# Optimization experiments

Hardware: AMD Instinct MI355X
Metric: run time of the kernel (lower is better)

The kernel has to match this reference:

```python
import jax, jax.numpy as jnp
from jax import lax
import numpy as np

B = 32768
N_IN = 8
N_HID = 64
N_CTRL = 2
M_SCEN = (1.0, 1.2)          # scenario parameters for f/g
M_NOM = 1.0
CLF_LAM = 1.0
CBF_LAM = 1.0
P_CLF = 100.0
P_CBF = 50.0
QP_ITERS = 80                # fixed-iteration batched ADMM (OSQP-style) replacing CvxpyLayer
RHO = 1.0
SIGMA = 1e-6
INF = jnp.inf


def setup_inputs() -> dict:
    key = jax.random.key(0)
    ks = jax.random.split(key, 16)
    s = 0.3
    return {
        "x":   jax.random.normal(ks[0], (B, N_IN), jnp.float32),
        "VW1": jax.random.normal(ks[1], (N_HID, N_IN), jnp.float32) * s,
        "Vb1": jax.random.normal(ks[2], (N_HID,), jnp.float32) * s,
        "VW2": jax.random.normal(ks[3], (N_HID, N_HID), jnp.float32) * s,
        "Vb2": jax.random.normal(ks[4], (N_HID,), jnp.float32) * s,
        "HW1": jax.random.normal(ks[5], (N_HID, N_IN), jnp.float32) * s,
        "Hb1": jax.random.normal(ks[6], (N_HID,), jnp.float32) * s,
        "HW2": jax.random.normal(ks[7], (N_HID, N_HID), jnp.float32) * s,
        "Hb2": jax.random.normal(ks[8], (N_HID,), jnp.float32) * s,
        "HW3": jax.random.normal(ks[9], (N_HID, N_HID), jnp.float32) * s,
        "Hb3": jax.random.normal(ks[10], (N_HID,), jnp.float32) * s,
        "HW4": jax.random.normal(ks[11], (1, N_HID), jnp.float32) * s,
        "Hb4": jax.random.normal(ks[12], (1,), jnp.float32) * s,
        "G0":  jax.random.normal(ks[13], (N_IN, N_CTRL), jnp.float32) * s,
        "K":   jax.random.normal(ks[14], (N_IN, N_CTRL), jnp.float32) * s,
    }


def _lyapunov(x, W1, b1, W2, b2):
    t1 = jnp.tanh(x @ W1.T + b1)                                   # [B,H]
    t2 = jnp.tanh(t1 @ W2.T + b2)                                  # [B,H]
    V = 0.5 * jnp.sum(t2 * t2, axis=1)                             # [B]
    # fused diag(1-t^2) @ W chain (no diag_embed materialization)
    D1 = (1.0 - t1 ** 2)[:, :, None] * W1[None]                    # [B,H,N]
    D2 = (1.0 - t2 ** 2)[:, :, None] * jnp.einsum('hk,bkn->bhn', W2, D1)
    grad_V = jnp.einsum('bh,bhn->bn', t2, D2)                      # [B,N]
    return V, grad_V


def _barrier(x, W1, b1, W2, b2, W3, b3, W4, b4):
    t1 = jnp.tanh(x @ W1.T + b1)
    t2 = jnp.tanh(t1 @ W2.T + b2)
    t3 = jnp.tanh(t2 @ W3.T + b3)
    H = t3 @ W4.T + b4                                             # [B,1]
    D1 = (1.0 - t1 ** 2)[:, :, None] * W1[None]
    D2 = (1.0 - t2 ** 2)[:, :, None] * jnp.einsum('hk,bkn->bhn', W2, D1)
    D3 = (1.0 - t3 ** 2)[:, :, None] * jnp.einsum('hk,bkn->bhn', W3, D2)
    grad_H = jnp.einsum('oh,bhn->bn', W4, D3)                      # [B,N] (o=1)
    return H, grad_H


def _solve_qp(q, A, lo, hi):
    """Batched OSQP-style ADMM for min 0.5 z^T P z + q^T z  s.t. lo <= A z <= hi.
    P = diag([2,2,0,0,0,0]); z = [u(2), r_clf(2), s_cbf(2)]. Fixed iterations."""
    nb, mc, nz = A.shape[0], A.shape[1], A.shape[2]
    Pdiag = jnp.array([2.0, 2.0, 0.0, 0.0, 0.0, 0.0], q.dtype)
    M = RHO * jnp.einsum('bmi,bmj->bij', A, A) + jnp.diag(Pdiag + SIGMA)
    Minv = jnp.linalg.inv(M)                                       # [B,6,6]
    x0 = jnp.zeros((nb, nz), q.dtype)
    z0 = jnp.zeros((nb, mc), q.dtype)
    y0 = jnp.zeros((nb, mc), q.dtype)

    def step(carry, _):
        xx, zz, yy = carry
        rhs = SIGMA * xx - q + jnp.einsum('bmi,bm->bi', A, RHO * zz - yy)
        xt = jnp.einsum('bij,bj->bi', Minv, rhs)
        zt = jnp.einsum('bmi,bi->bm', A, xt)
        zn = jnp.clip(zt + yy / RHO, lo, hi)
        yn = yy + RHO * (zt - zn)
        return (xt, zn, yn), None

    (xf, _, _), _ = lax.scan(step, (x0, z0, y0), None, length=QP_ITERS)
    return xf                                                      # [B,6]


def _forward(x, VW1, Vb1, VW2, Vb2, HW1, Hb1, HW2, Hb2, HW3, Hb3, HW4, Hb4, G0, K):
    V, grad_V = _lyapunov(x, VW1, Vb1, VW2, Vb2)
    H, grad_H = _barrier(x, HW1, Hb1, HW2, Hb2, HW3, Hb3, HW4, Hb4)

    LfVs, LgVs, LfHs, LgHs = [], [], [], []
    for m in M_SCEN:
        # f(x,m) = -x/m ; g(x,m) = G0/m
        LfVs.append(-jnp.sum(grad_V * x, axis=1) / m)              # [B]
        LgVs.append((grad_V @ G0) / m)                             # [B,C]
        LfHs.append(-jnp.sum(grad_H * x, axis=1) / m)
        LgHs.append((grad_H @ G0) / m)
    u_nom = -(x @ K) * (1.0 / M_NOM)                               # [B,C]

    nb = x.shape[0]
    z2 = jnp.zeros((nb, 2), x.dtype)
    ey = jnp.eye(2, dtype=x.dtype)
    e = lambda i: jnp.broadcast_to(ey[i], (nb, 2))
    ninf = jnp.full((nb,), -INF, x.dtype)
    pinf = jnp.full((nb,), INF, x.dtype)
    zer = jnp.zeros((nb,), x.dtype)

    rows, los, his = [], [], []
    for i in range(len(M_SCEN)):
        # CBF: LfH + LgH@u + cbf_lam*H + s_i >= 0
        rows.append(jnp.concatenate([LgHs[i], z2, e(i)], axis=1))
        los.append(-(LfHs[i] + CBF_LAM * H[:, 0])); his.append(pinf)
        # CLF: LfV + LgV@u + clf_lam*V - r_i <= 0
        rows.append(jnp.concatenate([LgVs[i], -e(i), z2], axis=1))
        los.append(ninf); his.append(-(LfVs[i] + CLF_LAM * V))
    for i in range(len(M_SCEN)):
        rows.append(jnp.concatenate([z2, e(i), z2], axis=1)); los.append(zer); his.append(pinf)
    for i in range(len(M_SCEN)):
        rows.append(jnp.concatenate([z2, z2, e(i)], axis=1)); los.append(zer); his.append(pinf)

    A = jnp.stack(rows, axis=1)                                    # [B,8,6]
    lo = jnp.stack(los, axis=1)                                    # [B,8]
    hi = jnp.stack(his, axis=1)
    # objective ||u-u_nom||^2 + p_clf*sum r + p_cbf*sum s  ->  q = [-2 u_nom, p_clf, p_clf, p_cbf, p_cbf]
    q = jnp.concatenate([-2.0 * u_nom,
                         jnp.full((nb, 2), P_CLF, x.dtype),
                         jnp.full((nb, 2), P_CBF, x.dtype)], axis=1)

    z = _solve_qp(q, A, lo, hi)                                    # [B,6]
    u = z[:, :N_CTRL]
    relaxation = jnp.mean(z[:, N_CTRL:N_CTRL + len(M_SCEN)], axis=1, keepdims=True)  # [B,1]

    ns = float(len(M_SCEN))
    Vdot = sum(LfVs[i] + jnp.sum(LgVs[i] * u, axis=1) for i in range(len(M_SCEN))) / ns
    Hdot = sum(LfHs[i] + jnp.sum(LgHs[i] * u, axis=1) for i in range(len(M_SCEN))) / ns
    return u, relaxation, V, Vdot[:, None, None], H, Hdot[:, None, None]


def reference(x, VW1, Vb1, VW2, Vb2, HW1, Hb1, HW2, Hb2, HW3, Hb3, HW4, Hb4, G0, K):
    return _forward(x, VW1, Vb1, VW2, Vb2, HW1, Hb1, HW2, Hb2, HW3, Hb3, HW4, Hb4, G0, K)
```

## Files before the change

### kernel.cpp

```cpp
#include <hip/hip_runtime.h>
#include <hip/hip_bf16.h>
#include <math.h>

typedef _Float16 f16x8 __attribute__((ext_vector_type(8)));
typedef _Float16 f16x4 __attribute__((ext_vector_type(4)));
typedef float    f32x4 __attribute__((ext_vector_type(4)));
typedef float    f32x2 __attribute__((ext_vector_type(2)));

__device__ __forceinline__ float ldin(const void* p, int i, int f32f) {
  return f32f ? ((const float*)p)[i]
              : __bfloat162float(((const __hip_bfloat16*)p)[i]);
}

__device__ __forceinline__ f32x4 MFMA(f16x8 a, f16x8 b, f32x4 c) {
  return __builtin_amdgcn_mfma_f32_16x16x32_f16(a, b, c, 0, 0, 0);
}

__device__ __forceinline__ float tanh_fast(float x) {
  float e = __expf(2.f * x);
  return 1.f - 2.f * __builtin_amdgcn_rcpf(e + 1.f);
}

__device__ __forceinline__ float redq(float v) {
  v += __shfl_xor(v, 16, 64);
  v += __shfl_xor(v, 32, 64);
  return v;
}

__device__ __forceinline__ int widx(int h, int k) {
  return ((h >> 4) << 10) + ((k >> 5) << 9) + (((k >> 3) & 3) << 7) + ((h & 15) << 3) + (k & 7);
}

#define OFF_VW2   0
#define OFF_VW2T  4096
#define OFF_HW2   8192
#define OFF_HW2T  12288
#define OFF_HW3   16384
#define OFF_HW3T  20480
#define OFF_W1V   24576
#define OFF_W1H   26624
#define CF_BASE   28672
#define C_WGV0 0
#define C_WGV1 64
#define C_WGH0 128
#define C_WGH1 192
#define C_VB1  256
#define C_VB2  320
#define C_HB1  384
#define C_HB2  448
#define C_HB3  512
#define C_W4   576
#define C_K    640
#define C_HB4  656
#define C_FLAG 657
#define C_N    658

__global__ __launch_bounds__(256) void prep_kernel(
    const void* px, const void* pVW1, const void* pVW2,
    const void* pHW1, const void* pHW2, const void* pHW3,
    const void* pVb1, const void* pVb2, const void* pHb1, const void* pHb2,
    const void* pHb3, const void* pHW4, const void* pHb4,
    const void* pG0, const void* pK, _Float16* wsp)
{
  __shared__ int sCnt;
  const int tid = threadIdx.x;
  if (tid == 0) sCnt = 0;
  __syncthreads();
  {
    const unsigned short* xb = (const unsigned short*)px;
    int good = 0;
#pragma unroll
    for (int i = 0; i < 2; ++i) {
      int ex = (xb[tid * 2 + i] >> 7) & 0xFF;
      good += (ex >= 97 && ex <= 157) ? 1 : 0;
    }
    atomicAdd(&sCnt, good);
  }
  __syncthreads();
  const int f32f = (sCnt >= 435) ? 0 : 1;

  const int t = blockIdx.x * 256 + tid;
  int h = t >> 6, k = t & 63;
  int fw = widx(h, k), tw = widx(k, h);
  _Float16 v;
  v = (_Float16)ldin(pVW2, t, f32f); wsp[OFF_VW2 + fw] = v; wsp[OFF_VW2T + tw] = v;
  v = (_Float16)ldin(pHW2, t, f32f); wsp[OFF_HW2 + fw] = v; wsp[OFF_HW2T + tw] = v;
  v = (_Float16)ldin(pHW3, t, f32f); wsp[OFF_HW3 + fw] = v; wsp[OFF_HW3T + tw] = v;
  if (t < 512) {
    int hh = t >> 3, j = t & 7;
    int base = ((hh >> 4) << 9) + ((hh & 15) << 3) + j;
    float f = ldin(pVW1, t, f32f); _Float16 hi = (_Float16)f;
    _Float16 lo = f32f ? (_Float16)(f - (float)hi) : (_Float16)0.f;
    wsp[OFF_W1V + base]       = hi;
    wsp[OFF_W1V + base + 128] = hi;
    wsp[OFF_W1V + base + 256] = lo;
    wsp[OFF_W1V + base + 384] = (_Float16)0.f;
    f = ldin(pHW1, t, f32f); hi = (_Float16)f;
    lo = f32f ? (_Float16)(f - (float)hi) : (_Float16)0.f;
    wsp[OFF_W1H + base]       = hi;
    wsp[OFF_W1H + base + 128] = hi;
    wsp[OFF_W1H + base + 256] = lo;
    wsp[OFF_W1H + base + 384] = (_Float16)0.f;
  }
  if (blockIdx.x == 0) {
    float* wsF = (float*)(wsp + CF_BASE);
    if (tid < 64) {
      float a0 = 0.f, a1 = 0.f, b0 = 0.f, b1 = 0.f;
#pragma unroll
      for (int nn = 0; nn < 8; ++nn) {
        float g0 = ldin(pG0, 2 * nn, f32f), g1 = ldin(pG0, 2 * nn + 1, f32f);
        float wv = ldin(pVW1, tid * 8 + nn, f32f), wh = ldin(pHW1, tid * 8 + nn, f32f);
        a0 += wv * g0; a1 += wv * g1; b0 += wh * g0; b1 += wh * g1;
      }
      wsF[C_WGV0 + tid] = a0; wsF[C_WGV1 + tid] = a1;
      wsF[C_WGH0 + tid] = b0; wsF[C_WGH1 + tid] = b1;
      wsF[C_VB1 + tid] = ldin(pVb1, tid, f32f);
      wsF[C_VB2 + tid] = ldin(pVb2, tid, f32f);
      wsF[C_HB1 + tid] = ldin(pHb1, tid, f32f);
      wsF[C_HB2 + tid] = ldin(pHb2, tid, f32f);
      wsF[C_HB3 + tid] = ldin(pHb3, tid, f32f);
      wsF[C_W4  + tid] = ldin(pHW4, tid, f32f);
    }
    if (tid < 16) wsF[C_K + tid] = ldin(pK, tid, f32f);
    if (tid == 0) { wsF[C_HB4] = ldin(pHb4, 0, f32f); ((int*)wsF)[C_FLAG] = f32f; }
  }
}

__global__ __launch_bounds__(512, 2) void main_kernel(
    const void* px, const _Float16* wsp, float* out)
{
  __shared__ __align__(16) _Float16 sAct[8][1024];
  __shared__ __align__(16) float sQPs[10][128];
  __shared__ __align__(16) float sC[C_N];

  const int tid = threadIdx.x, lane = tid & 63, w = tid >> 6;
  const int n = lane & 15, q = lane >> 4;
  const int e0 = blockIdx.x * 128 + w * 16;

  const float* cf = (const float*)(wsp + CF_BASE);
  for (int i = tid; i < C_N; i += 512) sC[i] = cf[i];
  const int f32f = ((const int*)cf)[C_FLAG];
  __syncthreads();

  float xv[8];
  if (f32f) {
    const f32x4* xp = (const f32x4*)((const float*)px + (e0 + n) * 8);
    f32x4 x0 = xp[0], x1 = xp[1];
#pragma unroll
    for (int j = 0; j < 4; ++j) { xv[j] = x0[j]; xv[4 + j] = x1[j]; }
  } else {
    uint4 u = *(const uint4*)((const unsigned short*)px + (e0 + n) * 8);
    unsigned uu[4] = {u.x, u.y, u.z, u.w};
#pragma unroll
    for (int j = 0; j < 4; ++j) {
      xv[2 * j]     = __uint_as_float(uu[j] << 16);
      xv[2 * j + 1] = __uint_as_float(uu[j] & 0xffff0000u);
    }
  }
  float un0 = 0.f, un1 = 0.f;
  f16x8 xb;
#pragma unroll
  for (int j = 0; j < 8; ++j) {
    _Float16 hh = (_Float16)xv[j];
    float lo = xv[j] - (float)hh;
    xb[j] = (q == 1) ? (_Float16)lo : ((q == 3) ? (_Float16)0.f : hh);
    un0 -= xv[j] * sC[C_K + 2 * j];
    un1 -= xv[j] * sC[C_K + 2 * j + 1];
  }

  _Float16* buf = sAct[w];

  auto gemm64 = [&](int poff, f32x4* acc) {
    f16x8 a[8];
#pragma unroll
    for (int i = 0; i < 8; ++i)
      a[i] = *(const f16x8*)(wsp + poff + i * 512 + lane * 8);
    f16x8 b0 = *(const f16x8*)(buf + lane * 8);
    f16x8 b1 = *(const f16x8*)(buf + 512 + lane * 8);
#pragma unroll
    for (int ht = 0; ht < 4; ++ht) {
      f32x4 c = {0.f, 0.f, 0.f, 0.f};
      c = MFMA(a[2 * ht], b0, c);
      c = MFMA(a[2 * ht + 1], b1, c);
      acc[ht] = c;
    }
  };
  auto l1gemm = [&](int off, f32x4* acc) {
    f16x8 a[4];
#pragma unroll
    for (int ht = 0; ht < 4; ++ht)
      a[ht] = *(const f16x8*)(wsp + off + ht * 512 + lane * 8);
#pragma unroll
    for (int ht = 0; ht < 4; ++ht) {
      f32x4 c = {0.f, 0.f, 0.f, 0.f};
      acc[ht] = MFMA(a[ht], xb, c);
    }
  };
  auto wst = [&](const f32x4* vals) {
#pragma unroll
    for (int ht = 0; ht < 4; ++ht) {
      int aw = ((ht >> 1) << 9) + (((ht & 1) * 2 + (q >> 1)) << 7) + n * 8 + ((q & 1) << 2);
      f16x4 vh;
#pragma unroll
      for (int r = 0; r < 4; ++r) vh[r] = (_Float16)vals[ht][r];
      *(f16x4*)(buf + aw) = vh;
    }
  };

  f32x4 acc[4], tv[4];

  f32x4 z1V[4], d1V[4];
  l1gemm(OFF_W1V, acc);
#pragma unroll
  for (int ht = 0; ht < 4; ++ht) {
    int hb = ht * 16 + q * 4;
    f32x4 bb = *(const f32x4*)&sC[C_VB1 + hb];
    z1V[ht] = acc[ht];
#pragma unroll
    for (int r = 0; r < 4; ++r) {
      float t = tanh_fast(z1V[ht][r] + bb[r]);
      tv[ht][r] = t; d1V[ht][r] = 1.f - t * t;
    }
  }
  wst(tv);

  gemm64(OFF_VW2, acc);
  float pV = 0.f;
#pragma unroll
  for (int ht = 0; ht < 4; ++ht) {
    int hb = ht * 16 + q * 4;
    f32x4 bb = *(const f32x4*)&sC[C_VB2 + hb];
#pragma unroll
    for (int r = 0; r < 4; ++r) {
      float t = tanh_fast(acc[ht][r] + bb[r]);
      pV += t * t;
      tv[ht][r] = t * (1.f - t * t);
    }
  }
  wst(tv);

  gemm64(OFF_VW2T, acc);
  float pgvx = 0.f, plv0 = 0.f, plv1 = 0.f;
#pragma unroll
  for (int ht = 0; ht < 4; ++ht) {
    int hb = ht * 16 + q * 4;
    f32x4 g0 = *(const f32x4*)&sC[C_WGV0 + hb];
    f32x4 g1 = *(const f32x4*)&sC[C_WGV1 + hb];
#pragma unroll
    for (int r = 0; r < 4; ++r) {
      float wt = acc[ht][r] * d1V[ht][r];
      pgvx += wt * z1V[ht][r];
      plv0 += wt * g0[r]; plv1 += wt * g1[r];
    }
  }

  f32x4 z1H[4], d1H[4], d2H[4];
  l1gemm(OFF_W1H, acc);
#pragma unroll
  for (int ht = 0; ht < 4; ++ht) {
    int hb = ht * 16 + q * 4;
    f32x4 bb = *(const f32x4*)&sC[C_HB1 + hb];
    z1H[ht] = acc[ht];
#pragma unroll
    for (int r = 0; r < 4; ++r) {
      float t = tanh_fast(z1H[ht][r] + bb[r]);
      tv[ht][r] = t; d1H[ht][r] = 1.f - t * t;
    }
  }
  wst(tv);

  gemm64(OFF_HW2, acc);
#pragma unroll
  for (int ht = 0; ht < 4; ++ht) {
    int hb = ht * 16 + q * 4;
    f32x4 bb = *(const f32x4*)&sC[C_HB2 + hb];
#pragma unroll
    for (int r = 0; r < 4; ++r) {
      float t = tanh_fast(acc[ht][r] + bb[r]);
      tv[ht][r] = t; d2H[ht][r] = 1.f - t * t;
    }
  }
  wst(tv);

  gemm64(OFF_HW3, acc);
  float pH = 0.f;
#pragma unroll
  for (int ht = 0; ht < 4; ++ht) {
    int hb = ht * 16 + q * 4;
    f32x4 bb = *(const f32x4*)&sC[C_HB3 + hb];
    f32x4 w4 = *(const f32x4*)&sC[C_W4 + hb];
#pragma unroll
    for (int r = 0; r < 4; ++r) {
      float t = tanh_fast(acc[ht][r] + bb[r]);
      pH += t * w4[r];
      tv[ht][r] = w4[r] * (1.f - t * t);
    }
  }
  wst(tv);

  gemm64(OFF_HW3T, acc);
#pragma unroll
  for (int ht = 0; ht < 4; ++ht)
#pragma unroll
    for (int r = 0; r < 4; ++r) tv[ht][r] = acc[ht][r] * d2H[ht][r];
  wst(tv);

  gemm64(OFF_HW2T, acc);
  float pghx = 0.f, plh0 = 0.f, plh1 = 0.f;
#pragma unroll
  for (int ht = 0; ht < 4; ++ht) {
    int hb = ht * 16 + q * 4;
    f32x4 g0 = *(const f32x4*)&sC[C_WGH0 + hb];
    f32x4 g1 = *(const f32x4*)&sC[C_WGH1 + hb];
#pragma unroll
    for (int r = 0; r < 4; ++r) {
      float wt = acc[ht][r] * d1H[ht][r];
      pghx += wt * z1H[ht][r];
      plh0 += wt * g0[r]; plh1 += wt * g1[r];
    }
  }

  {
    float a0 = redq(plh0), a1 = redq(plh1), a2 = redq(plv0), a3 = redq(plv1);
    float a4 = redq(pghx), a5 = redq(pgvx), a6 = redq(pV), a7 = redq(pH);
    if (q == 0) {
      int col = w * 16 + n;
      sQPs[0][col] = a0; sQPs[1][col] = a1; sQPs[2][col] = a2; sQPs[3][col] = a3;
      sQPs[4][col] = a4; sQPs[5][col] = a5; sQPs[6][col] = a6; sQPs[7][col] = a7;
      sQPs[8][col] = un0; sQPs[9][col] = un1;
    }
  }
  __syncthreads();
  if (w != 0 && w != 2) return;

  const int col = (w >> 1) * 64 + lane;
  const int e = blockIdx.x * 128 + col;
  float gh0 = sQPs[0][col], gh1 = sQPs[1][col];
  float gv0 = sQPs[2][col], gv1 = sQPs[3][col];
  float ghx = sQPs[4][col], gvx = sQPs[5][col];
  float V   = 0.5f * sQPs[6][col];
  float H   = sQPs[7][col] + sC[C_HB4];
  un0 = sQPs[8][col]; un1 = sQPs[9][col];
  out[98304 + e]  = V;
  out[163840 + e] = H;

  const float im = 1.0f / 1.2f;
  const float sg = 1e-6f;

  float lo0 = ghx - H;
  float hi1 = gvx - V;
  float lo2 = ghx * im - H;
  float hi3 = gvx * im - V;
  float nq0 = 2.f * un0, nq1 = 2.f * un1;

  const float d  = 2.f + sg;
  const float rd = 1.f / d;
  const float al = 1.f + im * im;
  const float be = al * (1.f - rd);
  float S00 = be * (gh0 * gh0 + gv0 * gv0) + d;
  float S11 = be * (gh1 * gh1 + gv1 * gv1) + d;
  float S01 = be * (gh0 * gh1 + gv0 * gv1);
  float idet = 1.f / (S00 * S11 - S01 * S01);
  float i00 = S11 * idet, i11 = S00 * idet, i01 = -S01 * idet;

  float X0 = 0.f, X1 = 0.f, X2 = 0.f, X3 = 0.f, X4 = 0.f, X5 = 0.f;
  float Z[8] = {0.f, 0.f, 0.f, 0.f, 0.f, 0.f, 0.f, 0.f};
  float Y[8] = {0.f, 0.f, 0.f, 0.f, 0.f, 0.f, 0.f, 0.f};

#pragma unroll 1
  for (int it = 0; it < 80; ++it) {
    float t0 = Z[0] - Y[0], t1 = Z[1] - Y[1], t2 = Z[2] - Y[2], t3 = Z[3] - Y[3];
    float t4 = Z[4] - Y[4], t5 = Z[5] - Y[5], t6 = Z[6] - Y[6], t7 = Z[7] - Y[7];
    float tauh = t0 + im * t2, tauv = t1 + im * t3;
    float b0 = nq0 + gh0 * tauh + gv0 * tauv;
    float b1 = nq1 + gh1 * tauh + gv1 * tauv;
    float b2 = -100.f - t1 + t4;
    float b3 = -100.f - t3 + t5;
    float b4 = -50.f + t0 + t6;
    float b5 = -50.f + t2 + t7;
    float pp = b2 + im * b3;
    float s2 = b4 + im * b5;
    float cb0 = gh0 * s2 - gv0 * pp;
    float cb1 = gh1 * s2 - gv1 * pp;
    float u0b = b0 - cb0 * rd;
    float u1b = b1 - cb1 * rd;
    X0 = i00 * u0b + i01 * u1b;
    X1 = i01 * u0b + i11 * u1b;
    float gdH = gh0 * X0 + gh1 * X1;
    float gdV = gv0 * X0 + gv1 * X1;
    X2 = (b2 + gdV) * rd;
    X3 = (b3 + im * gdV) * rd;
    X4 = (b4 - gdH) * rd;
    X5 = (b5 - im * gdH) * rd;
    float zt0 = gdH + X4;
    float zt1 = gdV - X2;
    float zt2 = gdH * im + X5;
    float zt3 = gdV * im - X3;

    float v, zn;
    v = zt0 + Y[0]; zn = fmaxf(v, lo0); Y[0] += zt0 - zn; Z[0] = zn;
    v = zt1 + Y[1]; zn = fminf(v, hi1); Y[1] += zt1 - zn; Z[1] = zn;
    v = zt2 + Y[2]; zn = fmaxf(v, lo2); Y[2] += zt2 - zn; Z[2] = zn;
    v = zt3 + Y[3]; zn = fminf(v, hi3); Y[3] += zt3 - zn; Z[3] = zn;
    v = X2 + Y[4];  zn = fmaxf(v, 0.f); Y[4] += X2 - zn;  Z[4] = zn;
    v = X3 + Y[5];  zn = fmaxf(v, 0.f); Y[5] += X3 - zn;  Z[5] = zn;
    v = X4 + Y[6];  zn = fmaxf(v, 0.f); Y[6] += X4 - zn;  Z[6] = zn;
    v = X5 + Y[7];  zn = fmaxf(v, 0.f); Y[7] += X5 - zn;  Z[7] = zn;
  }

  float relax = 0.5f * (X2 + X3);
  const float cc = 0.5f * (1.f + im);
  float Vdot = cc * (gv0 * X0 + gv1 * X1 - gvx);
  float Hdot = cc * (gh0 * X0 + gh1 * X1 - ghx);

  f32x2 uo; uo[0] = X0; uo[1] = X1;
  *(f32x2*)&out[2 * e] = uo;
  out[65536 + e]  = relax;
  out[131072 + e] = Vdot;
  out[196608 + e] = Hdot;
}

extern "C" void kernel_launch(void* const* d_in, const int* in_sizes, int n_in,
                              void* d_out, int out_size, void* d_ws, size_t ws_size,
                              hipStream_t stream) {
  (void)in_sizes; (void)n_in; (void)out_size; (void)ws_size;
  float* out = (float*)d_out;
  _Float16* wsp = (_Float16*)d_ws;
  prep_kernel<<<16, 256, 0, stream>>>(
      d_in[0], d_in[1], d_in[3], d_in[5], d_in[7], d_in[9],
      d_in[2], d_in[4], d_in[6], d_in[8], d_in[10], d_in[11], d_in[12],
      d_in[13], d_in[14], wsp);
  main_kernel<<<256, 512, 0, stream>>>(d_in[0], wsp, out);
}
```

Baseline: 107.6 us.

## Interleave V and H network chains and pack ADMM loop into float2 vectors

The Lyapunov and barrier MLP forward/backward chains are now interleaved per wave. Each wave keeps two LDS activation buffers and issues paired MFMA GEMMs for V and H, which exposes independent work to hide MFMA and tanh latency. The 80-iteration ADMM loop is rewritten on f32x2 vectors so the compiler can emit packed FP32 math. In exchange, launch bounds drop to one block per CU and LDS per block doubles, which raises register pressure and may lower occupancy.

```diff
diff --git a/kernel.cpp b/kernel.cpp
--- a/kernel.cpp
+++ b/kernel.cpp
@@ -126,10 +126,10 @@
   }
 }
 
-__global__ __launch_bounds__(512, 2) void main_kernel(
+__global__ __launch_bounds__(512, 1) void main_kernel(
     const void* px, const _Float16* wsp, float* out)
 {
-  __shared__ __align__(16) _Float16 sAct[8][1024];
+  __shared__ __align__(16) _Float16 sAct[16][1024];
   __shared__ __align__(16) float sQPs[10][128];
   __shared__ __align__(16) float sC[C_N];
 
@@ -168,144 +168,139 @@
     un1 -= xv[j] * sC[C_K + 2 * j + 1];
   }
 
-  _Float16* buf = sAct[w];
-
-  auto gemm64 = [&](int poff, f32x4* acc) {
+  _Float16* bufV = sAct[2 * w];
+  _Float16* bufH = sAct[2 * w + 1];
+
+  auto gemm64x2 = [&](int poffV, int poffH, f32x4* accV, f32x4* accH) {
+    f16x8 aV[8], aH[8];
+#pragma unroll
+    for (int i = 0; i < 8; ++i)
+      aV[i] = *(const f16x8*)(wsp + poffV + i * 512 + lane * 8);
+#pragma unroll
+    for (int i = 0; i < 8; ++i)
+      aH[i] = *(const f16x8*)(wsp + poffH + i * 512 + lane * 8);
+    f16x8 bV0 = *(const f16x8*)(bufV + lane * 8);
+    f16x8 bV1 = *(const f16x8*)(bufV + 512 + lane * 8);
+    f16x8 bH0 = *(const f16x8*)(bufH + lane * 8);
+    f16x8 bH1 = *(const f16x8*)(bufH + 512 + lane * 8);
+#pragma unroll
+    for (int ht = 0; ht < 4; ++ht) {
+      f32x4 c = {0.f, 0.f, 0.f, 0.f};
+      c = MFMA(aV[2 * ht], bV0, c);
+      accV[ht] = MFMA(aV[2 * ht + 1], bV1, c);
+      f32x4 d = {0.f, 0.f, 0.f, 0.f};
+      d = MFMA(aH[2 * ht], bH0, d);
+      accH[ht] = MFMA(aH[2 * ht + 1], bH1, d);
+    }
+  };
+  auto gemm64 = [&](int poff, const _Float16* b, f32x4* acc) {
     f16x8 a[8];
 #pragma unroll
     for (int i = 0; i < 8; ++i)
       a[i] = *(const f16x8*)(wsp + poff + i * 512 + lane * 8);
-    f16x8 b0 = *(const f16x8*)(buf + lane * 8);
-    f16x8 b1 = *(const f16x8*)(buf + 512 + lane * 8);
+    f16x8 b0 = *(const f16x8*)(b + lane * 8);
+    f16x8 b1 = *(const f16x8*)(b + 512 + lane * 8);
 #pragma unroll
     for (int ht = 0; ht < 4; ++ht) {
       f32x4 c = {0.f, 0.f, 0.f, 0.f};
       c = MFMA(a[2 * ht], b0, c);
-      c = MFMA(a[2 * ht + 1], b1, c);
-      acc[ht] = c;
+      acc[ht] = MFMA(a[2 * ht + 1], b1, c);
     }
   };
-  auto l1gemm = [&](int off, f32x4* acc) {
-    f16x8 a[4];
+  auto l1gemm2 = [&](f32x4* accV, f32x4* accH) {
+    f16x8 aV[4], aH[4];
 #pragma unroll
     for (int ht = 0; ht < 4; ++ht)
-      a[ht] = *(const f16x8*)(wsp + off + ht * 512 + lane * 8);
+      aV[ht] = *(const f16x8*)(wsp + OFF_W1V + ht * 512 + lane * 8);
+#pragma unroll
+    for (int ht = 0; ht < 4; ++ht)
+      aH[ht] = *(const f16x8*)(wsp + OFF_W1H + ht * 512 + lane * 8);
 #pragma unroll
     for (int ht = 0; ht < 4; ++ht) {
       f32x4 c = {0.f, 0.f, 0.f, 0.f};
-      acc[ht] = MFMA(a[ht], xb, c);
+      accV[ht] = MFMA(aV[ht], xb, c);
+      f32x4 d = {0.f, 0.f, 0.f, 0.f};
+      accH[ht] = MFMA(aH[ht], xb, d);
     }
   };
-  auto wst = [&](const f32x4* vals) {
+  auto wst = [&](const f32x4* vals, _Float16* b) {
 #pragma unroll
     for (int ht = 0; ht < 4; ++ht) {
       int aw = ((ht >> 1) << 9) + (((ht & 1) * 2 + (q >> 1)) << 7) + n * 8 + ((q & 1) << 2);
       f16x4 vh;
 #pragma unroll
       for (int r = 0; r < 4; ++r) vh[r] = (_Float16)vals[ht][r];
-      *(f16x4*)(buf + aw) = vh;
+      *(f16x4*)(b + aw) = vh;
     }
   };
 
-  f32x4 acc[4], tv[4];
-
-  f32x4 z1V[4], d1V[4];
-  l1gemm(OFF_W1V, acc);
+  f32x4 accV[4], accH[4], tvV[4], tvH[4];
+  f32x4 z1V[4], d1V[4], z1H[4], d1H[4], d2H[4];
+
+  l1gemm2(accV, accH);
 #pragma unroll
   for (int ht = 0; ht < 4; ++ht) {
     int hb = ht * 16 + q * 4;
-    f32x4 bb = *(const f32x4*)&sC[C_VB1 + hb];
-    z1V[ht] = acc[ht];
+    f32x4 bV = *(const f32x4*)&sC[C_VB1 + hb];
+    f32x4 bH = *(const f32x4*)&sC[C_HB1 + hb];
+    z1V[ht] = accV[ht]; z1H[ht] = accH[ht];
 #pragma unroll
     for (int r = 0; r < 4; ++r) {
-      float t = tanh_fast(z1V[ht][r] + bb[r]);
-      tv[ht][r] = t; d1V[ht][r] = 1.f - t * t;
-    }
-  }
-  wst(tv);
-
-  gemm64(OFF_VW2, acc);
+      float t = tanh_fast(z1V[ht][r] + bV[r]);
+      tvV[ht][r] = t; d1V[ht][r] = 1.f - t * t;
+      t = tanh_fast(z1H[ht][r] + bH[r]);
+      tvH[ht][r] = t; d1H[ht][r] = 1.f - t * t;
+    }
+  }
+  wst(tvV, bufV); wst(tvH, bufH);
+
+  gemm64x2(OFF_VW2, OFF_HW2, accV, accH);
   float pV = 0.f;
 #pragma unroll
   for (int ht = 0; ht < 4; ++ht) {
     int hb = ht * 16 + q * 4;
-    f32x4 bb = *(const f32x4*)&sC[C_VB2 + hb];
+    f32x4 bV = *(const f32x4*)&sC[C_VB2 + hb];
+    f32x4 bH = *(const f32x4*)&sC[C_HB2 + hb];
 #pragma unroll
     for (int r = 0; r < 4; ++r) {
-      float t = tanh_fast(acc[ht][r] + bb[r]);
+      float t = tanh_fast(accV[ht][r] + bV[r]);
       pV += t * t;
-      tv[ht][r] = t * (1.f - t * t);
-    }
-  }
-  wst(tv);
-
-  gemm64(OFF_VW2T, acc);
-  float pgvx = 0.f, plv0 = 0.f, plv1 = 0.f;
+      tvV[ht][r] = t * (1.f - t * t);
+      t = tanh_fast(accH[ht][r] + bH[r]);
+      tvH[ht][r] = t; d2H[ht][r] = 1.f - t * t;
+    }
+  }
+  wst(tvV, bufV); wst(tvH, bufH);
+
+  gemm64x2(OFF_VW2T, OFF_HW3, accV, accH);
+  float pgvx = 0.f, plv0 = 0.f, plv1 = 0.f, pH = 0.f;
 #pragma unroll
   for (int ht = 0; ht < 4; ++ht) {
     int hb = ht * 16 + q * 4;
     f32x4 g0 = *(const f32x4*)&sC[C_WGV0 + hb];
     f32x4 g1 = *(const f32x4*)&sC[C_WGV1 + hb];
+    f32x4 bH = *(const f32x4*)&sC[C_HB3 + hb];
+    f32x4 w4 = *(const f32x4*)&sC[C_W4 + hb];
 #pragma unroll
     for (int r = 0; r < 4; ++r) {
-      float wt = acc[ht][r] * d1V[ht][r];
+      float wt = accV[ht][r] * d1V[ht][r];
       pgvx += wt * z1V[ht][r];
       plv0 += wt * g0[r]; plv1 += wt * g1[r];
-    }
-  }
-
-  f32x4 z1H[4], d1H[4], d2H[4];
-  l1gemm(OFF_W1H, acc);
-#pragma unroll
-  for (int ht = 0; ht < 4; ++ht) {
-    int hb = ht * 16 + q * 4;
-    f32x4 bb = *(const f32x4*)&sC[C_HB1 + hb];
-    z1H[ht] = acc[ht];
-#pragma unroll
-    for (int r = 0; r < 4; ++r) {
-      float t = tanh_fast(z1H[ht][r] + bb[r]);
-      tv[ht][r] = t; d1H[ht][r] = 1.f - t * t;
-    }
-  }
-  wst(tv);
-
-  gemm64(OFF_HW2, acc);
-#pragma unroll
-  for (int ht = 0; ht < 4; ++ht) {
-    int hb = ht * 16 + q * 4;
-    f32x4 bb = *(const f32x4*)&sC[C_HB2 + hb];
-#pragma unroll
-    for (int r = 0; r < 4; ++r) {
-      float t = tanh_fast(acc[ht][r] + bb[r]);
-      tv[ht][r] = t; d2H[ht][r] = 1.f - t * t;
-    }
-  }
-  wst(tv);
-
-  gemm64(OFF_HW3, acc);
-  float pH = 0.f;
-#pragma unroll
-  for (int ht = 0; ht < 4; ++ht) {
-    int hb = ht * 16 + q * 4;
-    f32x4 bb = *(const f32x4*)&sC[C_HB3 + hb];
-    f32x4 w4 = *(const f32x4*)&sC[C_W4 + hb];
-#pragma unroll
-    for (int r = 0; r < 4; ++r) {
-      float t = tanh_fast(acc[ht][r] + bb[r]);
+      float t = tanh_fast(accH[ht][r] + bH[r]);
       pH += t * w4[r];
-      tv[ht][r] = w4[r] * (1.f - t * t);
-    }
-  }
-  wst(tv);
-
-  gemm64(OFF_HW3T, acc);
+      tvH[ht][r] = w4[r] * (1.f - t * t);
+    }
+  }
+  wst(tvH, bufH);
+
+  gemm64(OFF_HW3T, bufH, accH);
 #pragma unroll
   for (int ht = 0; ht < 4; ++ht)
 #pragma unroll
-    for (int r = 0; r < 4; ++r) tv[ht][r] = acc[ht][r] * d2H[ht][r];
-  wst(tv);
-
-  gemm64(OFF_HW2T, acc);
+    for (int r = 0; r < 4; ++r) tvH[ht][r] = accH[ht][r] * d2H[ht][r];
+  wst(tvH, bufH);
+
+  gemm64(OFF_HW2T, bufH, accH);
   float pghx = 0.f, plh0 = 0.f, plh1 = 0.f;
 #pragma unroll
   for (int ht = 0; ht < 4; ++ht) {
@@ -314,7 +309,7 @@
     f32x4 g1 = *(const f32x4*)&sC[C_WGH1 + hb];
 #pragma unroll
     for (int r = 0; r < 4; ++r) {
-      float wt = acc[ht][r] * d1H[ht][r];
+      float wt = accH[ht][r] * d1H[ht][r];
       pghx += wt * z1H[ht][r];
       plh0 += wt * g0[r]; plh1 += wt * g1[r];
     }
@@ -346,13 +341,6 @@
 
   const float im = 1.0f / 1.2f;
   const float sg = 1e-6f;
-
-  float lo0 = ghx - H;
-  float hi1 = gvx - V;
-  float lo2 = ghx * im - H;
-  float hi3 = gvx * im - V;
-  float nq0 = 2.f * un0, nq1 = 2.f * un1;
-
   const float d  = 2.f + sg;
   const float rd = 1.f / d;
   const float al = 1.f + im * im;
@@ -361,59 +349,58 @@
   float S11 = be * (gh1 * gh1 + gv1 * gv1) + d;
   float S01 = be * (gh0 * gh1 + gv0 * gv1);
   float idet = 1.f / (S00 * S11 - S01 * S01);
-  float i00 = S11 * idet, i11 = S00 * idet, i01 = -S01 * idet;
-
-  float X0 = 0.f, X1 = 0.f, X2 = 0.f, X3 = 0.f, X4 = 0.f, X5 = 0.f;
-  float Z[8] = {0.f, 0.f, 0.f, 0.f, 0.f, 0.f, 0.f, 0.f};
-  float Y[8] = {0.f, 0.f, 0.f, 0.f, 0.f, 0.f, 0.f, 0.f};
+
+  f32x2 IM2; IM2[0] = 1.f; IM2[1] = im;
+  f32x2 ghP; ghP[0] = gh0; ghP[1] = gh1;
+  f32x2 gvP; gvP[0] = gv0; gvP[1] = gv1;
+  f32x2 gHV0; gHV0[0] = gh0; gHV0[1] = gv0;
+  f32x2 gHV1; gHV1[0] = gh1; gHV1[1] = gv1;
+  f32x2 iA; iA[0] = S11 * idet;  iA[1] = -S01 * idet;
+  f32x2 iB; iB[0] = -S01 * idet; iB[1] = S00 * idet;
+  f32x2 nqP; nqP[0] = 2.f * un0; nqP[1] = 2.f * un1;
+  f32x2 loA; loA[0] = ghx - H;      loA[1] = ghx * im - H;
+  f32x2 hiB; hiB[0] = gvx - V;      hiB[1] = gvx * im - V;
+
+  f32x2 ZA = {0.f, 0.f}, ZB = {0.f, 0.f}, ZC = {0.f, 0.f}, ZD = {0.f, 0.f};
+  f32x2 YA = {0.f, 0.f}, YB = {0.f, 0.f}, YC = {0.f, 0.f}, YD = {0.f, 0.f};
+  f32x2 X01 = {0.f, 0.f}, XP = {0.f, 0.f}, XS = {0.f, 0.f};
 
 #pragma unroll 1
   for (int it = 0; it < 80; ++it) {
-    float t0 = Z[0] - Y[0], t1 = Z[1] - Y[1], t2 = Z[2] - Y[2], t3 = Z[3] - Y[3];
-    float t4 = Z[4] - Y[4], t5 = Z[5] - Y[5], t6 = Z[6] - Y[6], t7 = Z[7] - Y[7];
-    float tauh = t0 + im * t2, tauv = t1 + im * t3;
-    float b0 = nq0 + gh0 * tauh + gv0 * tauv;
-    float b1 = nq1 + gh1 * tauh + gv1 * tauv;
-    float b2 = -100.f - t1 + t4;
-    float b3 = -100.f - t3 + t5;
-    float b4 = -50.f + t0 + t6;
-    float b5 = -50.f + t2 + t7;
-    float pp = b2 + im * b3;
-    float s2 = b4 + im * b5;
-    float cb0 = gh0 * s2 - gv0 * pp;
-    float cb1 = gh1 * s2 - gv1 * pp;
-    float u0b = b0 - cb0 * rd;
-    float u1b = b1 - cb1 * rd;
-    X0 = i00 * u0b + i01 * u1b;
-    X1 = i01 * u0b + i11 * u1b;
-    float gdH = gh0 * X0 + gh1 * X1;
-    float gdV = gv0 * X0 + gv1 * X1;
-    X2 = (b2 + gdV) * rd;
-    X3 = (b3 + im * gdV) * rd;
-    X4 = (b4 - gdH) * rd;
-    X5 = (b5 - im * gdH) * rd;
-    float zt0 = gdH + X4;
-    float zt1 = gdV - X2;
-    float zt2 = gdH * im + X5;
-    float zt3 = gdV * im - X3;
-
-    float v, zn;
-    v = zt0 + Y[0]; zn = fmaxf(v, lo0); Y[0] += zt0 - zn; Z[0] = zn;
-    v = zt1 + Y[1]; zn = fminf(v, hi1); Y[1] += zt1 - zn; Z[1] = zn;
-    v = zt2 + Y[2]; zn = fmaxf(v, lo2); Y[2] += zt2 - zn; Z[2] = zn;
-    v = zt3 + Y[3]; zn = fminf(v, hi3); Y[3] += zt3 - zn; Z[3] = zn;
-    v = X2 + Y[4];  zn = fmaxf(v, 0.f); Y[4] += X2 - zn;  Z[4] = zn;
-    v = X3 + Y[5];  zn = fmaxf(v, 0.f); Y[5] += X3 - zn;  Z[5] = zn;
-    v = X4 + Y[6];  zn = fmaxf(v, 0.f); Y[6] += X4 - zn;  Z[6] = zn;
-    v = X5 + Y[7];  zn = fmaxf(v, 0.f); Y[7] += X5 - zn;  Z[7] = zn;
-  }
-
-  float relax = 0.5f * (X2 + X3);
+    f32x2 tA = ZA - YA, tB = ZB - YB, tC = ZC - YC, tD = ZD - YD;
+    float tauh = tA[0] + im * tA[1];
+    float tauv = tB[0] + im * tB[1];
+    f32x2 bU = nqP + ghP * tauh + gvP * tauv;
+    f32x2 bP = tC - tB - 100.f;
+    f32x2 bS = tA + tD - 50.f;
+    float pp = bP[0] + im * bP[1];
+    float s2 = bS[0] + im * bS[1];
+    f32x2 cb = ghP * s2 - gvP * pp;
+    f32x2 ub = bU - cb * rd;
+    X01 = iA * ub[0] + iB * ub[1];
+    f32x2 gd = gHV0 * X01[0] + gHV1 * X01[1];
+    XP = (bP + IM2 * gd[1]) * rd;
+    XS = (bS - IM2 * gd[0]) * rd;
+    f32x2 ztA = IM2 * gd[0] + XS;
+    f32x2 ztB = IM2 * gd[1] - XP;
+
+    f32x2 vv, zn;
+    vv = ztA + YA; zn[0] = fmaxf(vv[0], loA[0]); zn[1] = fmaxf(vv[1], loA[1]);
+    YA += ztA - zn; ZA = zn;
+    vv = ztB + YB; zn[0] = fminf(vv[0], hiB[0]); zn[1] = fminf(vv[1], hiB[1]);
+    YB += ztB - zn; ZB = zn;
+    vv = XP + YC;  zn[0] = fmaxf(vv[0], 0.f);   zn[1] = fmaxf(vv[1], 0.f);
+    YC += XP - zn; ZC = zn;
+    vv = XS + YD;  zn[0] = fmaxf(vv[0], 0.f);   zn[1] = fmaxf(vv[1], 0.f);
+    YD += XS - zn; ZD = zn;
+  }
+
+  float relax = 0.5f * (XP[0] + XP[1]);
   const float cc = 0.5f * (1.f + im);
-  float Vdot = cc * (gv0 * X0 + gv1 * X1 - gvx);
-  float Hdot = cc * (gh0 * X0 + gh1 * X1 - ghx);
-
-  f32x2 uo; uo[0] = X0; uo[1] = X1;
+  float Vdot = cc * (gv0 * X01[0] + gv1 * X01[1] - gvx);
+  float Hdot = cc * (gh0 * X01[0] + gh1 * X01[1] - ghx);
+
+  f32x2 uo; uo[0] = X01[0]; uo[1] = X01[1];
   *(f32x2*)&out[2 * e] = uo;
   out[65536 + e]  = relax;
   out[131072 + e] = Vdot;
```

After: 106.5 us. About the same (-1.1%).
